# Kernel optimization log

Hardware: AMD Instinct MI355X
Metric: run time of the kernel (lower is better)

Reference implementation:

```python
import jax, jax.numpy as jnp
import numpy as np

BS, NUM_EXPERTS, TOP_K = 2048, 64, 8
PROMPT_LEN, DIM = 32, 512


def setup_inputs() -> dict:
    key = jax.random.key(0)
    k1, k2, k3 = jax.random.split(key, 3)
    selection_score = jax.random.normal(k1, (BS, NUM_EXPERTS), dtype=jnp.float32)
    expert_indices = jax.random.randint(k2, (BS, TOP_K), 0, NUM_EXPERTS, dtype=jnp.int64)
    # torch.cat of num_experts Parameters each of shape [1, prompt_len, dim]
    all_weight = jax.random.normal(k3, (NUM_EXPERTS, PROMPT_LEN, DIM), dtype=jnp.float32)
    return {"selection_score": selection_score, "expert_indices": expert_indices, "all_weight": all_weight}


def reference(selection_score, expert_indices, all_weight):
    # gather selected expert prompts: [bs, top_k, prompt_len, dim]
    expert_prompt = all_weight[expert_indices]
    # gather matching routing scores: [bs, top_k]
    expert_scores = jnp.take_along_axis(selection_score, expert_indices, axis=1)
    # score-weighted sum over selected experts -> [bs, prompt_len, dim]
    mixture_prompt = jnp.einsum('bk,bkpd->bpd', expert_scores, expert_prompt)
    return mixture_prompt
```

## Files before the change

### kernel.cpp

```cpp
#include <hip/hip_runtime.h>


constexpr int BS  = 2048;
constexpr int NE  = 64;
constexpr int TK  = 8;
constexpr int PD  = 32 * 512;
constexpr int PD4 = PD / 4;

typedef float f32x4 __attribute__((ext_vector_type(4)));

__global__ __launch_bounds__(256) void moe_mix_kernel(
    const float* __restrict__ sel,
    const int*   __restrict__ idx,
    const float* __restrict__ W,
    float*       __restrict__ out)
{
    const int b = blockIdx.x;
    const int t = threadIdx.x;

    int   e[TK];
    float s[TK];
#pragma unroll
    for (int k = 0; k < TK; ++k) {
        e[k] = idx[b * TK + k];
        s[k] = sel[b * NE + e[k]];
    }

    const f32x4* __restrict__ W4 = reinterpret_cast<const f32x4*>(W);
    f32x4*       __restrict__ O4 = reinterpret_cast<f32x4*>(out) + (size_t)b * PD4;

#pragma unroll 2
    for (int j = 0; j < PD4 / 256; ++j) {
        const int f4 = t + j * 256;
        f32x4 acc = (f32x4)(0.f);
#pragma unroll
        for (int k = 0; k < TK; ++k) {
            const f32x4 w = W4[(size_t)e[k] * PD4 + f4];
            acc += s[k] * w;
        }
        __builtin_nontemporal_store(acc, &O4[f4]);
    }
}

extern "C" void kernel_launch(void* const* d_in, const int* in_sizes, int n_in,
                              void* d_out, int out_size, void* d_ws, size_t ws_size,
                              hipStream_t stream) {
    const float* sel = (const float*)d_in[0];
    const int*   idx = (const int*)d_in[1];
    const float* W   = (const float*)d_in[2];
    float*       out = (float*)d_out;

    moe_mix_kernel<<<dim3(BS), dim3(256), 0, stream>>>(sel, idx, W, out);
}
```

Before: 172.5 us.

## Stage bf16-converted expert weight tiles in LDS, reuse across row batches

```diff
diff --git a/kernel.cpp b/kernel.cpp
--- a/kernel.cpp
+++ b/kernel.cpp
@@ -1,44 +1,83 @@
 #include <hip/hip_runtime.h>
+#include <hip/hip_bf16.h>
 
 
-constexpr int BS  = 2048;
-constexpr int NE  = 64;
-constexpr int TK  = 8;
-constexpr int PD  = 32 * 512;
-constexpr int PD4 = PD / 4;
+constexpr int BS = 2048, NE = 64, TK = 8;
+constexpr int PD     = 32 * 512;
+constexpr int TILE   = 512;
+constexpr int NTILES = PD / TILE;
+constexpr int RPB    = 128;
+constexpr int NBB    = BS / RPB;
 
-typedef float f32x4 __attribute__((ext_vector_type(4)));
+typedef float          f32x4 __attribute__((ext_vector_type(4)));
+typedef unsigned short u16x4 __attribute__((ext_vector_type(4)));
+typedef unsigned short u16x8 __attribute__((ext_vector_type(8)));
 
-__global__ __launch_bounds__(256) void moe_mix_kernel(
+__global__ __launch_bounds__(256, 2) void moe_mix_lds(
     const float* __restrict__ sel,
     const int*   __restrict__ idx,
     const float* __restrict__ W,
     float*       __restrict__ out)
 {
-    const int b = blockIdx.x;
-    const int t = threadIdx.x;
+    __shared__ unsigned short w_lds[NE][TILE];
+    __shared__ int            i_lds[RPB][TK];
+    __shared__ float          s_lds[RPB][TK];
 
-    int   e[TK];
-    float s[TK];
+    const int tile = blockIdx.x & (NTILES - 1);
+    const int bb   = blockIdx.x / NTILES;
+    const int t    = threadIdx.x;
+
+    for (int i = t; i < NE * TILE / 4; i += 256) {
+        const int e  = i / (TILE / 4);
+        const int d4 = i % (TILE / 4);
+        const f32x4 w4 = *reinterpret_cast<const f32x4*>(
+            W + (size_t)e * PD + tile * TILE + d4 * 4);
+        u16x4 r;
 #pragma unroll
-    for (int k = 0; k < TK; ++k) {
-        e[k] = idx[b * TK + k];
-        s[k] = sel[b * NE + e[k]];
+        for (int j = 0; j < 4; ++j) {
+            __hip_bfloat16 h = __float2bfloat16(w4[j]);
+            r[j] = __builtin_bit_cast(unsigned short, h);
+        }
+        *reinterpret_cast<u16x4*>(&w_lds[e][d4 * 4]) = r;
     }
 
-    const f32x4* __restrict__ W4 = reinterpret_cast<const f32x4*>(W);
-    f32x4*       __restrict__ O4 = reinterpret_cast<f32x4*>(out) + (size_t)b * PD4;
+    {
+        const int4* src = reinterpret_cast<const int4*>(idx + (size_t)bb * RPB * TK);
+        int4*       dst = reinterpret_cast<int4*>(&i_lds[0][0]);
+        for (int i = t; i < RPB * TK / 4; i += 256) dst[i] = src[i];
+    }
+    __syncthreads();
 
-#pragma unroll 2
-    for (int j = 0; j < PD4 / 256; ++j) {
-        const int f4 = t + j * 256;
-        f32x4 acc = (f32x4)(0.f);
+    if (t < RPB) {
+        const int rg = bb * RPB + t;
+#pragma unroll
+        for (int k = 0; k < TK; ++k)
+            s_lds[t][k] = sel[(size_t)rg * NE + i_lds[t][k]];
+    }
+    __syncthreads();
+
+    const int wave = t >> 6;
+    const int lane = t & 63;
+    const int d0   = lane * 8;
+
+    for (int r = wave; r < RPB; r += 4) {
+        const int rg = bb * RPB + r;
+        f32x4 a0 = (f32x4)(0.f);
+        f32x4 a1 = (f32x4)(0.f);
 #pragma unroll
         for (int k = 0; k < TK; ++k) {
-            const f32x4 w = W4[(size_t)e[k] * PD4 + f4];
-            acc += s[k] * w;
+            const int   e = i_lds[r][k];
+            const float s = s_lds[r][k];
+            const u16x8 wv = *reinterpret_cast<const u16x8*>(&w_lds[e][d0]);
+#pragma unroll
+            for (int m = 0; m < 4; ++m) {
+                a0[m] += s * __builtin_bit_cast(float, ((unsigned)wv[m])     << 16);
+                a1[m] += s * __builtin_bit_cast(float, ((unsigned)wv[m + 4]) << 16);
+            }
         }
-        __builtin_nontemporal_store(acc, &O4[f4]);
+        float* op = out + (size_t)rg * PD + tile * TILE + d0;
+        *reinterpret_cast<f32x4*>(op)     = a0;
+        *reinterpret_cast<f32x4*>(op + 4) = a1;
     }
 }
 
@@ -50,5 +89,5 @@
     const float* W   = (const float*)d_in[2];
     float*       out = (float*)d_out;
 
-    moe_mix_kernel<<<dim3(BS), dim3(256), 0, stream>>>(sel, idx, W, out);
+    moe_mix_lds<<<dim3(NTILES * NBB), dim3(256), 0, stream>>>(sel, idx, W, out);
 }
```

Result: faster. 157.3 us (-8.8%).

## Reformulate MoE prompt mixing as dense bf16 MFMA GEMM with gate matrix

Applied to the files above, without the earlier changes.

```diff
diff --git a/kernel.cpp b/kernel.cpp
--- a/kernel.cpp
+++ b/kernel.cpp
@@ -1,43 +1,116 @@
 #include <hip/hip_runtime.h>
+#include <hip/hip_bf16.h>
 
 
-constexpr int BS  = 2048;
-constexpr int NE  = 64;
-constexpr int TK  = 8;
-constexpr int PD  = 32 * 512;
-constexpr int PD4 = PD / 4;
+constexpr int BS = 2048, NE = 64, TK = 8;
+constexpr int PD = 32 * 512;
 
-typedef float f32x4 __attribute__((ext_vector_type(4)));
+typedef float          f32x4 __attribute__((ext_vector_type(4)));
+typedef short          s16x8 __attribute__((ext_vector_type(8)));
+typedef unsigned short u16x4 __attribute__((ext_vector_type(4)));
+typedef unsigned short u16x8 __attribute__((ext_vector_type(8)));
 
-__global__ __launch_bounds__(256) void moe_mix_kernel(
-    const float* __restrict__ sel,
-    const int*   __restrict__ idx,
-    const float* __restrict__ W,
-    float*       __restrict__ out)
+__device__ __forceinline__ unsigned short f2bf(float f) {
+    __hip_bfloat16 h = __float2bfloat16(f);
+    return __builtin_bit_cast(unsigned short, h);
+}
+
+__global__ __launch_bounds__(256) void build_gate(
+    const float* __restrict__ sel, const int* __restrict__ idx,
+    unsigned short* __restrict__ G)
 {
-    const int b = blockIdx.x;
-    const int t = threadIdx.x;
+    const int b = blockIdx.x * 4 + (threadIdx.x >> 6);
+    const int e = threadIdx.x & 63;
+    int cnt = 0;
+#pragma unroll
+    for (int k = 0; k < TK; ++k) cnt += (idx[b * TK + k] == e) ? 1 : 0;
+    G[b * NE + e] = f2bf((float)cnt * sel[b * NE + e]);
+}
 
-    int   e[TK];
-    float s[TK];
+__global__ __launch_bounds__(256) void build_wt(
+    const float* __restrict__ W, unsigned short* __restrict__ Wt)
+{
+    __shared__ unsigned short lds[NE][128];
+    const int n0 = blockIdx.x * 128;
+    const int t  = threadIdx.x;
+
+    for (int i = t; i < NE * 32; i += 256) {
+        const int e = i >> 5, n4 = i & 31;
+        const f32x4 w = *reinterpret_cast<const f32x4*>(W + (size_t)e * PD + n0 + n4 * 4);
+        u16x4 r;
+#pragma unroll
+        for (int j = 0; j < 4; ++j) r[j] = f2bf(w[j]);
+        *reinterpret_cast<u16x4*>(&lds[e][n4 * 4]) = r;
+    }
+    __syncthreads();
+
+    if (t < 128) {
+        unsigned short* dst = Wt + (size_t)(n0 + t) * NE;
+#pragma unroll
+        for (int j = 0; j < 8; ++j) {
+            u16x8 v;
+#pragma unroll
+            for (int jj = 0; jj < 8; ++jj) v[jj] = lds[j * 8 + jj][t];
+            *reinterpret_cast<u16x8*>(dst + j * 8) = v;
+        }
+    }
+}
+
+__global__ __launch_bounds__(256) void gemm_moe(
+    const unsigned short* __restrict__ G,
+    const unsigned short* __restrict__ Wt,
+    float* __restrict__ out)
+{
+    const int t   = threadIdx.x;
+    const int w   = t >> 6, l = t & 63;
+    const int col = l & 15, kg = l >> 4;
+
+    const int bt  = blockIdx.x & 31;
+    const int nb  = blockIdx.x >> 5;
+    const int mb  = bt * 64 + w * 16;
+    const int nt0 = nb * 128;
+
+    const short* Gs  = reinterpret_cast<const short*>(G);
+    const short* Wts = reinterpret_cast<const short*>(Wt);
+
+    const s16x8 gb0 = *reinterpret_cast<const s16x8*>(Gs + (mb + col) * NE + 8 * kg);
+    const s16x8 gb1 = *reinterpret_cast<const s16x8*>(Gs + (mb + col) * NE + 32 + 8 * kg);
+
+#pragma unroll
+    for (int s = 0; s < 8; ++s) {
+        const int n0 = nt0 + s * 16;
+        const s16x8 a0 = *reinterpret_cast<const s16x8*>(
+            Wts + (size_t)(n0 + col) * NE + 8 * kg);
+        const s16x8 a1 = *reinterpret_cast<const s16x8*>(
+            Wts + (size_t)(n0 + col) * NE + 32 + 8 * kg);
+        f32x4 c = {0.f, 0.f, 0.f, 0.f};
+        c = __builtin_amdgcn_mfma_f32_16x16x32_bf16(a0, gb0, c, 0, 0, 0);
+        c = __builtin_amdgcn_mfma_f32_16x16x32_bf16(a1, gb1, c, 0, 0, 0);
+        __builtin_nontemporal_store(c, reinterpret_cast<f32x4*>(
+            out + (size_t)(mb + col) * PD + n0 + 4 * kg));
+    }
+}
+
+__global__ __launch_bounds__(256) void moe_mix_f32(
+    const float* __restrict__ sel, const int* __restrict__ idx,
+    const float* __restrict__ W, float* __restrict__ out)
+{
+    const int b = blockIdx.x, t = threadIdx.x;
+    int e[TK]; float s[TK];
 #pragma unroll
     for (int k = 0; k < TK; ++k) {
         e[k] = idx[b * TK + k];
         s[k] = sel[b * NE + e[k]];
     }
-
-    const f32x4* __restrict__ W4 = reinterpret_cast<const f32x4*>(W);
-    f32x4*       __restrict__ O4 = reinterpret_cast<f32x4*>(out) + (size_t)b * PD4;
-
+    const f32x4* W4 = reinterpret_cast<const f32x4*>(W);
+    f32x4*       O4 = reinterpret_cast<f32x4*>(out) + (size_t)b * (PD / 4);
 #pragma unroll 2
-    for (int j = 0; j < PD4 / 256; ++j) {
+    for (int j = 0; j < (PD / 4) / 256; ++j) {
         const int f4 = t + j * 256;
         f32x4 acc = (f32x4)(0.f);
 #pragma unroll
-        for (int k = 0; k < TK; ++k) {
-            const f32x4 w = W4[(size_t)e[k] * PD4 + f4];
-            acc += s[k] * w;
-        }
+        for (int k = 0; k < TK; ++k)
+            acc += s[k] * W4[(size_t)e[k] * (PD / 4) + f4];
         __builtin_nontemporal_store(acc, &O4[f4]);
     }
 }
@@ -50,5 +123,16 @@
     const float* W   = (const float*)d_in[2];
     float*       out = (float*)d_out;
 
-    moe_mix_kernel<<<dim3(BS), dim3(256), 0, stream>>>(sel, idx, W, out);
+    const size_t needG  = (size_t)BS * NE * sizeof(unsigned short);
+    const size_t needWt = (size_t)PD * NE * sizeof(unsigned short);
+
+    if (ws_size >= needG + needWt) {
+        unsigned short* G  = (unsigned short*)d_ws;
+        unsigned short* Wt = (unsigned short*)d_ws + (size_t)BS * NE;
+        build_gate<<<dim3(BS / 4), dim3(256), 0, stream>>>(sel, idx, G);
+        build_wt  <<<dim3(PD / 128), dim3(256), 0, stream>>>(W, Wt);
+        gemm_moe  <<<dim3(32 * 128), dim3(256), 0, stream>>>(G, Wt, out);
+    } else {
+        moe_mix_f32<<<dim3(BS), dim3(256), 0, stream>>>(sel, idx, W, out);
+    }
 }
```

After: 176.5 us. 1.02x slower.
